# Kernel tuning notes

Hardware: AMD Instinct MI355X
Metric: run time of the kernel (lower is better)

Reference implementation:

```python
import jax, jax.numpy as jnp
import numpy as np

NEG = -1e30  # stands in for -inf on the diagonal; exp(NEG - max) == 0 exactly


def setup_inputs() -> dict:
    key = jax.random.key(0)
    k1, k2, k3, k4, k5 = jax.random.split(key, 5)
    B, C, H, W = 4, 512, 128, 128
    mid = C // 8  # 64
    x = jax.random.normal(k1, (B, C, H, W), dtype=jnp.float32)
    Wq = jax.random.normal(k2, (mid, C), dtype=jnp.float32) * (1.0 / np.sqrt(C))
    Wk = jax.random.normal(k3, (mid, C), dtype=jnp.float32) * (1.0 / np.sqrt(C))
    Wv = jax.random.normal(k4, (C, C), dtype=jnp.float32) * (1.0 / np.sqrt(C))
    gamma = jax.random.normal(k5, (1,), dtype=jnp.float32) * 0.1
    return {"x": x, "Wq": Wq, "Wk": Wk, "Wv": Wv, "gamma": gamma}


def reference(x, Wq, Wk, Wv, gamma):
    B, C, H, W = x.shape
    # 1x1 convs == channel matmuls
    q = jnp.einsum('bchw,mc->bmhw', x, Wq)  # (B, mid, H, W)
    k = jnp.einsum('bchw,mc->bmhw', x, Wk)
    v = jnp.einsum('bchw,dc->bdhw', x, Wv)  # (B, C, H, W)

    # vertical (H-axis) logits with -inf diagonal: eH[b,i,w,j] = sum_m q[b,m,i,w] k[b,m,j,w]
    eH = jnp.einsum('bmiw,bmjw->biwj', q, k)           # (B, H, W, H)
    diag = jnp.eye(H, dtype=bool)[:, None, :]          # (H, 1, H)
    eH = jnp.where(diag, NEG, eH)

    # horizontal (W-axis) logits: eW[b,h,i,j] = sum_m q[b,m,h,i] k[b,m,h,j]
    eW = jnp.einsum('bmhi,bmhj->bhij', q, k)           # (B, H, W, W)

    # joint softmax over the concatenated H+W logits
    attn = jax.nn.softmax(jnp.concatenate([eH, eW], axis=3), axis=3)  # (B, H, W, H+W)
    aH = attn[:, :, :, :H]  # (B, H, W, H)
    aW = attn[:, :, :, H:]  # (B, H, W, W)

    # attention-weighted value aggregation along each axis
    outH = jnp.einsum('bcjw,biwj->bciw', v, aH)  # (B, C, H, W)
    outW = jnp.einsum('bchj,bhij->bchi', v, aW)  # (B, C, H, W)

    return gamma[0] * (outH + outW) + x
```

## Files before the change

### kernel.cpp

```cpp
#include <hip/hip_runtime.h>
#include <cstdint>
#include <cstddef>

#define NEGV (-1e30f)

constexpr int C_ = 512, H_ = 128, W_ = 128;
constexpr int P_ = 16384;

typedef short bf16x8 __attribute__((ext_vector_type(8)));
typedef float f32x4  __attribute__((ext_vector_type(4)));
#define MFMA16(a, b, c) __builtin_amdgcn_mfma_f32_16x16x32_bf16((a), (b), (c), 0, 0, 0)

#define SWZI(r, cu) ((((r) << 7)) + (((((cu) >> 3) ^ ((r) & 15))) << 3) + ((cu) & 7))

__device__ inline unsigned short f2bf(float f) {
    union { float f; uint32_t i; } t; t.f = f;
    uint32_t r = t.i + 0x7FFFu + ((t.i >> 16) & 1u);
    return (unsigned short)(r >> 16);
}
__device__ inline float bf2f(unsigned short u) {
    union { uint32_t i; float f; } t; t.i = (uint32_t)u << 16; return t.f;
}
__device__ inline uint32_t bfadd2(uint32_t a, uint32_t b) {
    union { uint32_t i; float f; } alo, ahi, blo, bhi;
    alo.i = a << 16; ahi.i = a & 0xffff0000u;
    blo.i = b << 16; bhi.i = b & 0xffff0000u;
    const float lo = alo.f + blo.f, hi = ahi.f + bhi.f;
    return (uint32_t)f2bf(lo) | ((uint32_t)f2bf(hi) << 16);
}
__device__ inline uint4 bfadd8(const uint4 a, const uint4 b) {
    uint4 r; r.x = bfadd2(a.x, b.x); r.y = bfadd2(a.y, b.y);
    r.z = bfadd2(a.z, b.z); r.w = bfadd2(a.w, b.w); return r;
}

__global__ __launch_bounds__(256) void kwconv(
    const float* __restrict__ Wq, const float* __restrict__ Wk,
    const float* __restrict__ Wv,
    unsigned short* __restrict__ Wqkbf, unsigned short* __restrict__ Wvbf)
{
    const int i4 = (blockIdx.x * 256 + threadIdx.x) * 4;
    const float* src; unsigned short* dst; int off;
    if (i4 < 32768)       { src = Wq + i4;          dst = Wqkbf + i4; }
    else if (i4 < 65536)  { off = i4 - 32768; src = Wk + off; dst = Wqkbf + i4; }
    else                  { off = i4 - 65536; src = Wv + off; dst = Wvbf + off; }
    const float4 v = *(const float4*)src;
    ushort4 u; u.x = f2bf(v.x); u.y = f2bf(v.y); u.z = f2bf(v.z); u.w = f2bf(v.w);
    *(ushort4*)dst = u;
}

__global__ __launch_bounds__(256) void kprep1(
    const float* __restrict__ x, unsigned short* __restrict__ xTbf)
{
    __shared__ float t[32][33];
    const int tx = threadIdx.x, ty = threadIdx.y;
    const int h0 = (blockIdx.x >> 2) * 32, w0 = (blockIdx.x & 3) * 32;
    const size_t base = (size_t)blockIdx.y * P_;
#pragma unroll
    for (int k = 0; k < 4; k++)
        t[ty + 8 * k][tx] = x[base + (size_t)(h0 + ty + 8 * k) * 128 + w0 + tx];
    __syncthreads();
#pragma unroll
    for (int k = 0; k < 4; k++)
        xTbf[base + (size_t)(w0 + ty + 8 * k) * 128 + h0 + tx] = f2bf(t[tx][ty + 8 * k]);
}

__global__ __launch_bounds__(256) void kprep2(
    const float* __restrict__ x, unsigned short* __restrict__ xbfT)
{
    __shared__ float t[32][33];
    const int tx = threadIdx.x, ty = threadIdx.y;
    const int p0 = blockIdx.x * 32, c0 = blockIdx.y * 32, b = blockIdx.z;
#pragma unroll
    for (int k = 0; k < 4; k++)
        t[ty + 8 * k][tx] = x[((size_t)(b * C_ + c0 + ty + 8 * k)) * P_ + p0 + tx];
    __syncthreads();
#pragma unroll
    for (int k = 0; k < 4; k++)
        xbfT[((size_t)b * P_ + p0 + ty + 8 * k) * C_ + c0 + tx] = f2bf(t[tx][ty + 8 * k]);
}

__global__ __launch_bounds__(256) void kgemm_mfma(
    const unsigned short* __restrict__ A, const unsigned short* __restrict__ Bm,
    const unsigned short* __restrict__ Bm2,
    unsigned short* __restrict__ outbf, float* __restrict__ outf,
    const float* __restrict__ addx, const float* __restrict__ gammap)
{
    __shared__ __attribute__((aligned(16))) unsigned short sA[128 * 72];
    __shared__ __attribute__((aligned(16))) unsigned short sB[128 * 72];
    const int tid = threadIdx.x;
    const int pbase = blockIdx.x * 128, mt = blockIdx.y, b = blockIdx.z;
    const int lane = tid & 63, wv = tid >> 6;
    const int m0 = (wv >> 1) * 64, p0 = (wv & 1) * 64;
    const int fr = lane & 15, fq = lane >> 4;

    f32x4 acc[4][4];
#pragma unroll
    for (int i = 0; i < 4; i++)
#pragma unroll
        for (int j = 0; j < 4; j++) acc[i][j] = (f32x4){0.f, 0.f, 0.f, 0.f};

    const size_t arow0 = (size_t)(mt * 128) * 512;
    const size_t brow0 = ((size_t)b * P_ + pbase) * 512;

    for (int kc = 0; kc < 512; kc += 64) {
#pragma unroll
        for (int rep = 0; rep < 4; rep++) {
            const int idx = rep * 256 + tid;
            const int kg = idx & 7, r = idx >> 3;
            *(uint4*)&sA[r * 72 + kg * 8] = *(const uint4*)&A[arow0 + (size_t)r * 512 + kc + kg * 8];
            const size_t boff = brow0 + (size_t)r * 512 + kc + kg * 8;
            uint4 vb = *(const uint4*)&Bm[boff];
            if (Bm2) vb = bfadd8(vb, *(const uint4*)&Bm2[boff]);
            *(uint4*)&sB[r * 72 + kg * 8] = vb;
        }
        __syncthreads();
#pragma unroll
        for (int kk = 0; kk < 64; kk += 32) {
            bf16x8 af[4], bfv[4];
#pragma unroll
            for (int t = 0; t < 4; t++) af[t]  = *(const bf16x8*)&sA[(m0 + t * 16 + fr) * 72 + kk + fq * 8];
#pragma unroll
            for (int t = 0; t < 4; t++) bfv[t] = *(const bf16x8*)&sB[(p0 + t * 16 + fr) * 72 + kk + fq * 8];
#pragma unroll
            for (int i = 0; i < 4; i++)
#pragma unroll
                for (int j = 0; j < 4; j++)
                    acc[i][j] = MFMA16(af[i], bfv[j], acc[i][j]);
        }
        __syncthreads();
    }

    if (outbf) {
#pragma unroll
        for (int tj = 0; tj < 4; tj++) {
            const int p_g = pbase + p0 + tj * 16 + fr;
            const size_t rowo = ((size_t)b * P_ + p_g) * 128;
#pragma unroll
            for (int ti = 0; ti < 4; ti++) {
                const int mk = m0 + ti * 16 + fq * 4;
                ushort4 u;
                u.x = f2bf(acc[ti][tj][0]); u.y = f2bf(acc[ti][tj][1]);
                u.z = f2bf(acc[ti][tj][2]); u.w = f2bf(acc[ti][tj][3]);
                *(ushort4*)&outbf[rowo + mk] = u;
            }
        }
    } else {
        const float g = gammap[0];
#pragma unroll
        for (int ti = 0; ti < 4; ti++)
#pragma unroll
            for (int r = 0; r < 4; r++) {
                const int m_g = mt * 128 + m0 + ti * 16 + fq * 4 + r;
                const size_t rowo = ((size_t)(b * 512 + m_g)) * P_;
#pragma unroll
                for (int tj = 0; tj < 4; tj++) {
                    const int p_g = pbase + p0 + tj * 16 + fr;
                    outf[rowo + p_g] = fmaf(g, acc[ti][tj][r], addx[rowo + p_g]);
                }
            }
    }
}

__global__ __launch_bounds__(256) void klogits(
    const unsigned short* __restrict__ qkP,
    float* __restrict__ ERow, float* __restrict__ ECol)
{
    __shared__ __attribute__((aligned(16))) unsigned short sPM[128 * 136];
    const int tid = threadIdx.x;
    const int s = blockIdx.x, b = blockIdx.y, mode = blockIdx.z;
    const int rowMul  = mode ? 1 : 128;
    const int rowStep = mode ? 128 : 1;
    float* E = mode ? ECol : ERow;
    const size_t qbase = (size_t)b * P_ * 128;
    const int rb = s * rowMul;
#pragma unroll
    for (int rep = 0; rep < 8; rep++) {
        const int idx = rep * 256 + tid;
        const int mkg = idx & 15, i = idx >> 4;
        *(uint4*)&sPM[i * 136 + mkg * 8] =
            *(const uint4*)&qkP[qbase + (size_t)(rb + i * rowStep) * 128 + mkg * 8];
    }
    __syncthreads();

    const int lane = tid & 63, wv = tid >> 6;
    const int i0 = (wv >> 1) * 64, j0 = (wv & 1) * 64;
    const int fr = lane & 15, fq = lane >> 4;

    f32x4 acc[4][4];
#pragma unroll
    for (int i = 0; i < 4; i++)
#pragma unroll
        for (int j = 0; j < 4; j++) acc[i][j] = (f32x4){0.f, 0.f, 0.f, 0.f};

#pragma unroll
    for (int kk = 0; kk < 64; kk += 32) {
        bf16x8 af[4], bfv[4];
#pragma unroll
        for (int t = 0; t < 4; t++) af[t]  = *(const bf16x8*)&sPM[(i0 + t * 16 + fr) * 136 + kk + fq * 8];
#pragma unroll
        for (int t = 0; t < 4; t++) bfv[t] = *(const bf16x8*)&sPM[(j0 + t * 16 + fr) * 136 + 64 + kk + fq * 8];
#pragma unroll
        for (int i = 0; i < 4; i++)
#pragma unroll
            for (int j = 0; j < 4; j++)
                acc[i][j] = MFMA16(af[i], bfv[j], acc[i][j]);
    }

    float* Eb = E + ((size_t)(b * 128 + s)) * P_;
#pragma unroll
    for (int ti = 0; ti < 4; ti++)
#pragma unroll
        for (int r = 0; r < 4; r++) {
            const int i_g = i0 + ti * 16 + fq * 4 + r;
#pragma unroll
            for (int tj = 0; tj < 4; tj++) {
                const int j_g = j0 + tj * 16 + fr;
                float v = acc[ti][tj][r];
                if (mode && i_g == j_g) v = NEGV;
                Eb[(size_t)i_g * 128 + j_g] = v;
            }
        }
}

__global__ __launch_bounds__(256) void ksoftmax(
    const float* __restrict__ ER, const float* __restrict__ EC,
    unsigned short* __restrict__ AR, unsigned short* __restrict__ AC)
{
    const int lane = threadIdx.x & 63;
    const int pix = blockIdx.x * 4 + (threadIdx.x >> 6);
    const int b = pix >> 14, rem = pix & 16383;
    const int h = rem >> 7, w = rem & 127;
    const size_t ro = ((size_t)((b * 128 + h) * 128 + w)) * 128;
    const size_t co = ((size_t)((b * 128 + w) * 128 + h)) * 128;
    const float2 r = *(const float2*)(ER + ro + lane * 2);
    const float2 c = *(const float2*)(EC + co + lane * 2);
    float mx = fmaxf(fmaxf(r.x, r.y), fmaxf(c.x, c.y));
#pragma unroll
    for (int off = 32; off > 0; off >>= 1) mx = fmaxf(mx, __shfl_xor(mx, off));
    const float e0 = __expf(r.x - mx), e1 = __expf(r.y - mx);
    const float e2 = __expf(c.x - mx), e3 = __expf(c.y - mx);
    float sm = e0 + e1 + e2 + e3;
#pragma unroll
    for (int off = 32; off > 0; off >>= 1) sm += __shfl_xor(sm, off);
    const float inv = 1.0f / sm;
    ushort2 u0; u0.x = f2bf(e0 * inv); u0.y = f2bf(e1 * inv);
    ushort2 u1; u1.x = f2bf(e2 * inv); u1.y = f2bf(e3 * inv);
    *(ushort2*)(AR + ro + lane * 2) = u0;
    *(ushort2*)(AC + co + lane * 2) = u1;
}

__global__ __launch_bounds__(256) void kagg2(
    const unsigned short* __restrict__ ARow, const unsigned short* __restrict__ ACol,
    const float* __restrict__ x, const unsigned short* __restrict__ xTbf,
    unsigned short* __restrict__ ySumR, unsigned short* __restrict__ ySumC)
{
    __shared__ __attribute__((aligned(16))) unsigned short sAttn[128 * 128];
    __shared__ __attribute__((aligned(16))) unsigned short sX[128 * 128];
    const int tid = threadIdx.x;
    const int s = blockIdx.x, b = blockIdx.y, mode = blockIdx.z;
    const int lane = tid & 63, wv = tid >> 6;
    const int m0 = (wv >> 1) * 64, n0 = (wv & 1) * 64;
    const int fr = lane & 15, fq = lane >> 4;

    const unsigned short* At = (mode ? ACol : ARow) + ((size_t)(b * 128 + s)) * P_;
#pragma unroll
    for (int rep = 0; rep < 8; rep++) {
        const int idx = rep * 256 + tid;
        const int jg = idx & 15, row = idx >> 4;
        *(uint4*)&sAttn[SWZI(row, jg * 8)] = *(const uint4*)&At[(size_t)row * 128 + jg * 8];
    }

    unsigned short* yS = mode ? ySumC : ySumR;

    for (int ct = 0; ct < 4; ct++) {
        if (mode == 0) {
#pragma unroll
            for (int rep = 0; rep < 16; rep++) {
                const int idx = rep * 256 + tid;
                const int jq = idx & 31, cc = idx >> 5;
                const float4 v = *(const float4*)&x[((size_t)(b * C_ + ct * 128 + cc)) * P_ + s * 128 + jq * 4];
                ushort4 u; u.x = f2bf(v.x); u.y = f2bf(v.y); u.z = f2bf(v.z); u.w = f2bf(v.w);
                *(ushort4*)&sX[SWZI(cc, jq * 4)] = u;
            }
        } else {
#pragma unroll
            for (int rep = 0; rep < 8; rep++) {
                const int idx = rep * 256 + tid;
                const int jg = idx & 15, cc = idx >> 4;
                *(uint4*)&sX[SWZI(cc, jg * 8)] =
                    *(const uint4*)&xTbf[((size_t)(b * C_ + ct * 128 + cc)) * P_ + s * 128 + jg * 8];
            }
        }
        __syncthreads();

        f32x4 acc[4][4];
#pragma unroll
        for (int i = 0; i < 4; i++)
#pragma unroll
            for (int j = 0; j < 4; j++) acc[i][j] = (f32x4){0.f, 0.f, 0.f, 0.f};

#pragma unroll
        for (int kk = 0; kk < 128; kk += 32) {
            bf16x8 af[4], bfv[4];
#pragma unroll
            for (int t = 0; t < 4; t++) af[t]  = *(const bf16x8*)&sX[SWZI(m0 + t * 16 + fr, kk + fq * 8)];
#pragma unroll
            for (int t = 0; t < 4; t++) bfv[t] = *(const bf16x8*)&sAttn[SWZI(n0 + t * 16 + fr, kk + fq * 8)];
#pragma unroll
            for (int i = 0; i < 4; i++)
#pragma unroll
                for (int j = 0; j < 4; j++)
                    acc[i][j] = MFMA16(af[i], bfv[j], acc[i][j]);
        }

        const int cg0 = ct * 128 + m0 + fq * 4;
#pragma unroll
        for (int tj = 0; tj < 4; tj++) {
            const int i_g = n0 + tj * 16 + fr;
            const size_t p = mode ? ((size_t)i_g * 128 + s) : ((size_t)s * 128 + i_g);
            unsigned short* rowp = yS + ((size_t)b * P_ + p) * 512;
#pragma unroll
            for (int ti = 0; ti < 4; ti++) {
                ushort4 u;
                u.x = f2bf(acc[ti][tj][0]); u.y = f2bf(acc[ti][tj][1]);
                u.z = f2bf(acc[ti][tj][2]); u.w = f2bf(acc[ti][tj][3]);
                *(ushort4*)&rowp[cg0 + ti * 16] = u;
            }
        }
        __syncthreads();
    }
}

extern "C" void kernel_launch(void* const* d_in, const int* in_sizes, int n_in,
                              void* d_out, int out_size, void* d_ws, size_t ws_size,
                              hipStream_t stream) {
    const float* x     = (const float*)d_in[0];
    const float* Wq    = (const float*)d_in[1];
    const float* Wk    = (const float*)d_in[2];
    const float* Wv    = (const float*)d_in[3];
    const float* gamma = (const float*)d_in[4];
    float* out = (float*)d_out;

    char* base = (char*)d_ws;
    unsigned short* Wqkbf = (unsigned short*)base;             base += 131072;
    unsigned short* Wvbf  = (unsigned short*)base;             base += 524288;
    unsigned short* xTbf  = (unsigned short*)base;             base += 67108864;
    unsigned short* xbfT  = (unsigned short*)base;             base += 67108864;
    unsigned short* qkP   = (unsigned short*)base;             base += 16777216;
    float*          ERow  = (float*)base;                      base += 33554432;
    float*          ECol  = (float*)base;                      base += 33554432;
    unsigned short* ARow  = (unsigned short*)base;             base += 16777216;
    unsigned short* ACol  = (unsigned short*)base;             base += 16777216;
    unsigned short* ySumR = (unsigned short*)base;             base += 67108864;
    unsigned short* ySumC = (unsigned short*)ERow;

    kwconv<<<320, 256, 0, stream>>>(Wq, Wk, Wv, Wqkbf, Wvbf);
    kprep1<<<dim3(16, 2048), dim3(32, 8), 0, stream>>>(x, xTbf);
    kprep2<<<dim3(512, 16, 4), dim3(32, 8), 0, stream>>>(x, xbfT);
    kgemm_mfma<<<dim3(128, 1, 4), 256, 0, stream>>>(Wqkbf, xbfT, nullptr, qkP, nullptr, nullptr, nullptr);
    klogits<<<dim3(128, 4, 2), 256, 0, stream>>>(qkP, ERow, ECol);
    ksoftmax<<<16384, 256, 0, stream>>>(ERow, ECol, ARow, ACol);
    kagg2<<<dim3(128, 4, 2), 256, 0, stream>>>(ARow, ACol, x, xTbf, ySumR, ySumC);
    kgemm_mfma<<<dim3(128, 4, 4), 256, 0, stream>>>(Wvbf, ySumR, ySumC, nullptr, out, x, gamma);
}
```

Measured before the change: 558.4 us.

## Split final GEMM with K-concatenation, direct-to-LDS loads and vectorized epilogue

Replaces the generic GEMM for the final projection with a dedicated kernel. It concatenates the row and column aggregations along K, which removes the bf16 add that rounded their sum. It stages tiles via global_load_lds with an XOR swizzle instead of padded LDS, and transposes the MFMA role so the epilogue writes float4 vectors along the pixel dimension. kagg2 also switches its bf16 loads to direct-to-LDS with a matching swizzle. The cost is twice the K iterations in the final GEMM, traded for cheaper loads and coalesced stores.

```diff
diff --git a/kernel.cpp b/kernel.cpp
--- a/kernel.cpp
+++ b/kernel.cpp
@@ -11,26 +11,19 @@
 typedef float f32x4  __attribute__((ext_vector_type(4)));
 #define MFMA16(a, b, c) __builtin_amdgcn_mfma_f32_16x16x32_bf16((a), (b), (c), 0, 0, 0)
 
-#define SWZI(r, cu) ((((r) << 7)) + (((((cu) >> 3) ^ ((r) & 15))) << 3) + ((cu) & 7))
+#define SWZ128(r, cs) (((r) << 7) + (((((cs) >> 3) ^ ((r) & 7))) << 3) + ((cs) & 7))
+#define SWZ64(r, cs)  (((r) << 6) + (((((cs) >> 3) ^ ((r) & 7))) << 3) + ((cs) & 7))
+
+__device__ inline void gl_lds16(const void* g, void* l) {
+    __builtin_amdgcn_global_load_lds(
+        (const __attribute__((address_space(1))) unsigned int*)g,
+        (__attribute__((address_space(3))) unsigned int*)l, 16, 0, 0);
+}
 
 __device__ inline unsigned short f2bf(float f) {
     union { float f; uint32_t i; } t; t.f = f;
     uint32_t r = t.i + 0x7FFFu + ((t.i >> 16) & 1u);
     return (unsigned short)(r >> 16);
-}
-__device__ inline float bf2f(unsigned short u) {
-    union { uint32_t i; float f; } t; t.i = (uint32_t)u << 16; return t.f;
-}
-__device__ inline uint32_t bfadd2(uint32_t a, uint32_t b) {
-    union { uint32_t i; float f; } alo, ahi, blo, bhi;
-    alo.i = a << 16; ahi.i = a & 0xffff0000u;
-    blo.i = b << 16; bhi.i = b & 0xffff0000u;
-    const float lo = alo.f + blo.f, hi = ahi.f + bhi.f;
-    return (uint32_t)f2bf(lo) | ((uint32_t)f2bf(hi) << 16);
-}
-__device__ inline uint4 bfadd8(const uint4 a, const uint4 b) {
-    uint4 r; r.x = bfadd2(a.x, b.x); r.y = bfadd2(a.y, b.y);
-    r.z = bfadd2(a.z, b.z); r.w = bfadd2(a.w, b.w); return r;
 }
 
 __global__ __launch_bounds__(256) void kwconv(
@@ -79,16 +72,14 @@
         xbfT[((size_t)b * P_ + p0 + ty + 8 * k) * C_ + c0 + tx] = f2bf(t[tx][ty + 8 * k]);
 }
 
-__global__ __launch_bounds__(256) void kgemm_mfma(
+__global__ __launch_bounds__(256) void kgemmqk(
     const unsigned short* __restrict__ A, const unsigned short* __restrict__ Bm,
-    const unsigned short* __restrict__ Bm2,
-    unsigned short* __restrict__ outbf, float* __restrict__ outf,
-    const float* __restrict__ addx, const float* __restrict__ gammap)
+    unsigned short* __restrict__ outbf)
 {
     __shared__ __attribute__((aligned(16))) unsigned short sA[128 * 72];
     __shared__ __attribute__((aligned(16))) unsigned short sB[128 * 72];
     const int tid = threadIdx.x;
-    const int pbase = blockIdx.x * 128, mt = blockIdx.y, b = blockIdx.z;
+    const int pbase = blockIdx.x * 128, b = blockIdx.z;
     const int lane = tid & 63, wv = tid >> 6;
     const int m0 = (wv >> 1) * 64, p0 = (wv & 1) * 64;
     const int fr = lane & 15, fq = lane >> 4;
@@ -99,7 +90,6 @@
 #pragma unroll
         for (int j = 0; j < 4; j++) acc[i][j] = (f32x4){0.f, 0.f, 0.f, 0.f};
 
-    const size_t arow0 = (size_t)(mt * 128) * 512;
     const size_t brow0 = ((size_t)b * P_ + pbase) * 512;
 
     for (int kc = 0; kc < 512; kc += 64) {
@@ -107,11 +97,8 @@
         for (int rep = 0; rep < 4; rep++) {
             const int idx = rep * 256 + tid;
             const int kg = idx & 7, r = idx >> 3;
-            *(uint4*)&sA[r * 72 + kg * 8] = *(const uint4*)&A[arow0 + (size_t)r * 512 + kc + kg * 8];
-            const size_t boff = brow0 + (size_t)r * 512 + kc + kg * 8;
-            uint4 vb = *(const uint4*)&Bm[boff];
-            if (Bm2) vb = bfadd8(vb, *(const uint4*)&Bm2[boff]);
-            *(uint4*)&sB[r * 72 + kg * 8] = vb;
+            *(uint4*)&sA[r * 72 + kg * 8] = *(const uint4*)&A[(size_t)r * 512 + kc + kg * 8];
+            *(uint4*)&sB[r * 72 + kg * 8] = *(const uint4*)&Bm[brow0 + (size_t)r * 512 + kc + kg * 8];
         }
         __syncthreads();
 #pragma unroll
@@ -130,34 +117,18 @@
         __syncthreads();
     }
 
-    if (outbf) {
-#pragma unroll
-        for (int tj = 0; tj < 4; tj++) {
-            const int p_g = pbase + p0 + tj * 16 + fr;
-            const size_t rowo = ((size_t)b * P_ + p_g) * 128;
-#pragma unroll
-            for (int ti = 0; ti < 4; ti++) {
-                const int mk = m0 + ti * 16 + fq * 4;
-                ushort4 u;
-                u.x = f2bf(acc[ti][tj][0]); u.y = f2bf(acc[ti][tj][1]);
-                u.z = f2bf(acc[ti][tj][2]); u.w = f2bf(acc[ti][tj][3]);
-                *(ushort4*)&outbf[rowo + mk] = u;
-            }
-        }
-    } else {
-        const float g = gammap[0];
-#pragma unroll
-        for (int ti = 0; ti < 4; ti++)
-#pragma unroll
-            for (int r = 0; r < 4; r++) {
-                const int m_g = mt * 128 + m0 + ti * 16 + fq * 4 + r;
-                const size_t rowo = ((size_t)(b * 512 + m_g)) * P_;
-#pragma unroll
-                for (int tj = 0; tj < 4; tj++) {
-                    const int p_g = pbase + p0 + tj * 16 + fr;
-                    outf[rowo + p_g] = fmaf(g, acc[ti][tj][r], addx[rowo + p_g]);
-                }
-            }
+#pragma unroll
+    for (int tj = 0; tj < 4; tj++) {
+        const int p_g = pbase + p0 + tj * 16 + fr;
+        const size_t rowo = ((size_t)b * P_ + p_g) * 128;
+#pragma unroll
+        for (int ti = 0; ti < 4; ti++) {
+            const int mk = m0 + ti * 16 + fq * 4;
+            ushort4 u;
+            u.x = f2bf(acc[ti][tj][0]); u.y = f2bf(acc[ti][tj][1]);
+            u.z = f2bf(acc[ti][tj][2]); u.w = f2bf(acc[ti][tj][3]);
+            *(ushort4*)&outbf[rowo + mk] = u;
+        }
     }
 }
 
@@ -266,29 +237,30 @@
 #pragma unroll
     for (int rep = 0; rep < 8; rep++) {
         const int idx = rep * 256 + tid;
-        const int jg = idx & 15, row = idx >> 4;
-        *(uint4*)&sAttn[SWZI(row, jg * 8)] = *(const uint4*)&At[(size_t)row * 128 + jg * 8];
+        const int r = idx >> 4, sl = idx & 15;
+        gl_lds16(&At[(size_t)r * 128 + (sl ^ (r & 7)) * 8], &sAttn[idx * 8]);
     }
 
     unsigned short* yS = mode ? ySumC : ySumR;
 
     for (int ct = 0; ct < 4; ct++) {
         if (mode == 0) {
+            const float* Xf = &x[((size_t)(b * C_ + ct * 128)) * P_ + s * 128];
 #pragma unroll
             for (int rep = 0; rep < 16; rep++) {
                 const int idx = rep * 256 + tid;
                 const int jq = idx & 31, cc = idx >> 5;
-                const float4 v = *(const float4*)&x[((size_t)(b * C_ + ct * 128 + cc)) * P_ + s * 128 + jq * 4];
+                const float4 v = *(const float4*)&Xf[(size_t)cc * P_ + jq * 4];
                 ushort4 u; u.x = f2bf(v.x); u.y = f2bf(v.y); u.z = f2bf(v.z); u.w = f2bf(v.w);
-                *(ushort4*)&sX[SWZI(cc, jq * 4)] = u;
+                *(ushort4*)&sX[SWZ128(cc, jq * 4)] = u;
             }
         } else {
+            const unsigned short* Xs = &xTbf[((size_t)(b * C_ + ct * 128)) * P_ + s * 128];
 #pragma unroll
             for (int rep = 0; rep < 8; rep++) {
                 const int idx = rep * 256 + tid;
-                const int jg = idx & 15, cc = idx >> 4;
-                *(uint4*)&sX[SWZI(cc, jg * 8)] =
-                    *(const uint4*)&xTbf[((size_t)(b * C_ + ct * 128 + cc)) * P_ + s * 128 + jg * 8];
+                const int r = idx >> 4, sl = idx & 15;
+                gl_lds16(&Xs[(size_t)r * P_ + (sl ^ (r & 7)) * 8], &sX[idx * 8]);
             }
         }
         __syncthreads();
@@ -303,9 +275,15 @@
         for (int kk = 0; kk < 128; kk += 32) {
             bf16x8 af[4], bfv[4];
 #pragma unroll
-            for (int t = 0; t < 4; t++) af[t]  = *(const bf16x8*)&sX[SWZI(m0 + t * 16 + fr, kk + fq * 8)];
-#pragma unroll
-            for (int t = 0; t < 4; t++) bfv[t] = *(const bf16x8*)&sAttn[SWZI(n0 + t * 16 + fr, kk + fq * 8)];
+            for (int t = 0; t < 4; t++) {
+                const int rc = m0 + t * 16 + fr;
+                af[t] = *(const bf16x8*)&sX[SWZ128(rc, kk + fq * 8)];
+            }
+#pragma unroll
+            for (int t = 0; t < 4; t++) {
+                const int ri = n0 + t * 16 + fr;
+                bfv[t] = *(const bf16x8*)&sAttn[SWZ128(ri, kk + fq * 8)];
+            }
 #pragma unroll
             for (int i = 0; i < 4; i++)
 #pragma unroll
@@ -328,6 +306,84 @@
             }
         }
         __syncthreads();
+    }
+}
+
+__global__ __launch_bounds__(256) void kfinal(
+    const unsigned short* __restrict__ Wvbf,
+    const unsigned short* __restrict__ yR,
+    const unsigned short* __restrict__ yC,
+    float* __restrict__ outf,
+    const float* __restrict__ addx,
+    const float* __restrict__ gammap)
+{
+    __shared__ __attribute__((aligned(16))) unsigned short sM[128 * 64];
+    __shared__ __attribute__((aligned(16))) unsigned short sP[128 * 64];
+    const int tid = threadIdx.x;
+    const int pbase = blockIdx.x * 128, mt = blockIdx.y, b = blockIdx.z;
+    const int lane = tid & 63, wv = tid >> 6;
+    const int p0 = (wv >> 1) * 64, m0 = (wv & 1) * 64;
+    const int fr = lane & 15, fq = lane >> 4;
+
+    f32x4 acc[4][4];
+#pragma unroll
+    for (int i = 0; i < 4; i++)
+#pragma unroll
+        for (int j = 0; j < 4; j++) acc[i][j] = (f32x4){0.f, 0.f, 0.f, 0.f};
+
+    const unsigned short* Arow = Wvbf + (size_t)(mt * 128) * 512;
+    const size_t brow = ((size_t)b * P_ + pbase) * 512;
+
+    for (int chunk = 0; chunk < 16; ++chunk) {
+        const int kc = (chunk & 7) * 64;
+        const unsigned short* Bp = (chunk < 8 ? yR : yC) + brow + kc;
+        const unsigned short* Ap = Arow + kc;
+        if (chunk) __syncthreads();
+#pragma unroll
+        for (int rep = 0; rep < 4; rep++) {
+            const int idx = rep * 256 + tid;
+            const int r = idx >> 3, kgs = (idx & 7) ^ (r & 7);
+            gl_lds16(&Ap[(size_t)r * 512 + kgs * 8], &sM[idx * 8]);
+            gl_lds16(&Bp[(size_t)r * 512 + kgs * 8], &sP[idx * 8]);
+        }
+        __syncthreads();
+#pragma unroll
+        for (int kk = 0; kk < 64; kk += 32) {
+            bf16x8 ap[4], am[4];
+#pragma unroll
+            for (int t = 0; t < 4; t++) {
+                const int rp = p0 + t * 16 + fr;
+                ap[t] = *(const bf16x8*)&sP[SWZ64(rp, kk + fq * 8)];
+            }
+#pragma unroll
+            for (int t = 0; t < 4; t++) {
+                const int rm = m0 + t * 16 + fr;
+                am[t] = *(const bf16x8*)&sM[SWZ64(rm, kk + fq * 8)];
+            }
+#pragma unroll
+            for (int i = 0; i < 4; i++)
+#pragma unroll
+                for (int j = 0; j < 4; j++)
+                    acc[i][j] = MFMA16(ap[i], am[j], acc[i][j]);
+        }
+    }
+
+    const float g = gammap[0];
+#pragma unroll
+    for (int ti = 0; ti < 4; ti++) {
+        const int p_g = pbase + p0 + ti * 16 + fq * 4;
+#pragma unroll
+        for (int tj = 0; tj < 4; tj++) {
+            const int m_g = mt * 128 + m0 + tj * 16 + fr;
+            const size_t off = ((size_t)(b * 512 + m_g)) * P_ + p_g;
+            const float4 xa = *(const float4*)&addx[off];
+            float4 o;
+            o.x = fmaf(g, acc[ti][tj][0], xa.x);
+            o.y = fmaf(g, acc[ti][tj][1], xa.y);
+            o.z = fmaf(g, acc[ti][tj][2], xa.z);
+            o.w = fmaf(g, acc[ti][tj][3], xa.w);
+            *(float4*)&outf[off] = o;
+        }
     }
 }
 
@@ -357,9 +413,9 @@
     kwconv<<<320, 256, 0, stream>>>(Wq, Wk, Wv, Wqkbf, Wvbf);
     kprep1<<<dim3(16, 2048), dim3(32, 8), 0, stream>>>(x, xTbf);
     kprep2<<<dim3(512, 16, 4), dim3(32, 8), 0, stream>>>(x, xbfT);
-    kgemm_mfma<<<dim3(128, 1, 4), 256, 0, stream>>>(Wqkbf, xbfT, nullptr, qkP, nullptr, nullptr, nullptr);
+    kgemmqk<<<dim3(128, 1, 4), 256, 0, stream>>>(Wqkbf, xbfT, qkP);
     klogits<<<dim3(128, 4, 2), 256, 0, stream>>>(qkP, ERow, ECol);
     ksoftmax<<<16384, 256, 0, stream>>>(ERow, ECol, ARow, ACol);
     kagg2<<<dim3(128, 4, 2), 256, 0, stream>>>(ARow, ACol, x, xTbf, ySumR, ySumC);
-    kgemm_mfma<<<dim3(128, 4, 4), 256, 0, stream>>>(Wvbf, ySumR, ySumC, nullptr, out, x, gamma);
-}
+    kfinal<<<dim3(128, 4, 4), 256, 0, stream>>>(Wvbf, ySumR, ySumC, out, x, gamma);
+}
```

Result: faster. 537.6 us (-3.7%).
